# Kernel tuning notes

Hardware: AMD Instinct MI355X
Metric: run time of the kernel (lower is better)

## Reference

```python
import jax, jax.numpy as jnp
import numpy as np

EPS = 1e-5

def _bn2d(x, gamma, beta):
    # training-mode BatchNorm2d: stats over (B, T, F) per channel, biased var
    m = x.mean(axis=(0, 2, 3), keepdims=True)
    v = x.var(axis=(0, 2, 3), keepdims=True)
    return (x - m) * jax.lax.rsqrt(v + EPS) * gamma[None, :, None, None] + beta[None, :, None, None]

def _gn1(x, gamma, beta):
    # GroupNorm(num_groups=1) on (B, C, T): stats over (C, T) per sample
    m = x.mean(axis=(1, 2), keepdims=True)
    v = x.var(axis=(1, 2), keepdims=True)
    return (x - m) * jax.lax.rsqrt(v + EPS) * gamma[None, :, None] + beta[None, :, None]

def _nearest(x, size):
    # torch F.interpolate(mode='nearest') on last dim: src = floor(dst * L_in / L_out)
    L = x.shape[-1]
    idx = jnp.floor(jnp.arange(size) * (L / size)).astype(jnp.int32)
    return x[..., idx]


def setup_inputs() -> dict:
    key = jax.random.key(0)
    ks = jax.random.split(key, 16)
    B, Ca, T, Fa = 2, 512, 256, 128
    Tv = 64
    d = {
        "audio": jax.random.normal(ks[0], (B, Ca, T, Fa), dtype=jnp.float32),
        "video_emb": jax.random.normal(ks[1], (B, Ca, Tv), dtype=jnp.float32),
        # value_conv: depthwise 1x1 Conv2d (no bias) + BatchNorm2d
        "value_w": jax.random.normal(ks[2], (Ca,), dtype=jnp.float32) * 0.1 + 1.0,
        "value_gamma": jax.random.normal(ks[3], (Ca,), dtype=jnp.float32) * 0.1 + 1.0,
        "value_beta": jax.random.normal(ks[4], (Ca,), dtype=jnp.float32) * 0.1,
        # gate_conv: depthwise 1x1 Conv2d (no bias) + BatchNorm2d + ReLU
        "gate_w": jax.random.normal(ks[5], (Ca,), dtype=jnp.float32) * 0.1 + 1.0,
        "gate_gamma": jax.random.normal(ks[6], (Ca,), dtype=jnp.float32) * 0.1 + 1.0,
        "gate_beta": jax.random.normal(ks[7], (Ca,), dtype=jnp.float32) * 0.1,
        # attention_conv: depthwise Conv1d (bias) + GroupNorm(1)
        "att_w": jax.random.normal(ks[8], (Ca,), dtype=jnp.float32) * 0.1 + 1.0,
        "att_b": jax.random.normal(ks[9], (Ca,), dtype=jnp.float32) * 0.1,
        "att_gamma": jax.random.normal(ks[10], (Ca,), dtype=jnp.float32) * 0.1 + 1.0,
        "att_beta": jax.random.normal(ks[11], (Ca,), dtype=jnp.float32) * 0.1,
        # resize_conv: depthwise Conv1d (bias) + GroupNorm(1)
        "res_w": jax.random.normal(ks[12], (Ca,), dtype=jnp.float32) * 0.1 + 1.0,
        "res_b": jax.random.normal(ks[13], (Ca,), dtype=jnp.float32) * 0.1,
        "res_gamma": jax.random.normal(ks[14], (Ca,), dtype=jnp.float32) * 0.1 + 1.0,
        "res_beta": jax.random.normal(ks[15], (Ca,), dtype=jnp.float32) * 0.1,
    }
    return d


def reference(audio, video_emb, value_w, value_gamma, value_beta,
              gate_w, gate_gamma, gate_beta,
              att_w, att_b, att_gamma, att_beta,
              res_w, res_b, res_gamma, res_beta):
    T = audio.shape[2]
    # value branch: depthwise 1x1 conv (per-channel scale) + BN
    a_v = _bn2d(audio * value_w[None, :, None, None], value_gamma, value_beta)  # (B,Ca,T,Fa)
    # attention from video: depthwise conv1d + GN(1) + softmax over time + nearest resize
    att = _gn1(video_emb * att_w[None, :, None] + att_b[None, :, None], att_gamma, att_beta)
    att = _nearest(jax.nn.softmax(att, axis=-1), T)  # (B,Ca,T)
    f1 = att[..., None] * a_v
    # gating branch
    vr = _gn1(video_emb * res_w[None, :, None] + res_b[None, :, None], res_gamma, res_beta)
    vi = _nearest(vr, T)[..., None]  # (B,Ca,T,1)
    a_gate = jax.nn.relu(_bn2d(audio * gate_w[None, :, None, None], gate_gamma, gate_beta))
    f2 = a_gate * vi
    return f1 + f2
```

## Files before the change

### kernel.cpp

```cpp
#include <hip/hip_runtime.h>
#include <math.h>

#define EPS 1e-5f

typedef float f32x4 __attribute__((ext_vector_type(4)));

constexpr int B   = 2;
constexpr int Ca  = 512;
constexpr int T   = 256;
constexpr int Fa  = 128;
constexpr int Tv  = 64;
constexpr int CHW = T * Fa;
constexpr int NSTAT = B * CHW;
constexpr int VID_PER_B = Ca * Tv;

constexpr int WS_COEF = 0;
constexpr int WS_PS   = 2048;
constexpr int WS_PS2  = 4096;
constexpr int WS_ATT  = 6144;
constexpr int WS_VR   = WS_ATT + B * VID_PER_B;

__global__ __launch_bounds__(256) void k_stats(
    const float* __restrict__ audio, float* __restrict__ ws)
{
    const int blk = blockIdx.x;
    const int tid = threadIdx.x;
    const f32x4* a4 = reinterpret_cast<const f32x4*>(audio) + (size_t)blk * 4096;

    float s = 0.f, s2 = 0.f;
    #pragma unroll
    for (int k = 0; k < 16; ++k) {
        f32x4 v = a4[tid + k * 256];
        s  += v.x + v.y + v.z + v.w;
        s2 += v.x * v.x + v.y * v.y + v.z * v.z + v.w * v.w;
    }
    for (int off = 32; off; off >>= 1) {
        s  += __shfl_xor(s,  off);
        s2 += __shfl_xor(s2, off);
    }
    __shared__ float ls[4], ls2[4];
    const int wid = tid >> 6;
    if ((tid & 63) == 0) { ls[wid] = s; ls2[wid] = s2; }
    __syncthreads();
    if (tid == 0) {
        ws[WS_PS  + blk] = ls[0]  + ls[1]  + ls[2]  + ls[3];
        ws[WS_PS2 + blk] = ls2[0] + ls2[1] + ls2[2] + ls2[3];
    }
}

__global__ __launch_bounds__(1024) void k_video(
    const float* __restrict__ video,
    const float* __restrict__ vw, const float* __restrict__ vg, const float* __restrict__ vb,
    const float* __restrict__ gw, const float* __restrict__ gg, const float* __restrict__ gb,
    const float* __restrict__ aw, const float* __restrict__ ab,
    const float* __restrict__ ag, const float* __restrict__ abeta,
    const float* __restrict__ rw, const float* __restrict__ rb,
    const float* __restrict__ rg, const float* __restrict__ rbeta,
    float* __restrict__ ws)
{
    const int b   = blockIdx.x;
    const int tid = threadIdx.x;

    if (b == 0 && tid < Ca) {
        const int c = tid;
        const float S  = ws[WS_PS  + c*2] + ws[WS_PS  + c*2 + 1]
                       + ws[WS_PS  + 1024 + c*2] + ws[WS_PS  + 1024 + c*2 + 1];
        const float S2 = ws[WS_PS2 + c*2] + ws[WS_PS2 + c*2 + 1]
                       + ws[WS_PS2 + 1024 + c*2] + ws[WS_PS2 + 1024 + c*2 + 1];
        const float inv  = 1.f / (float)NSTAT;
        const float mean = S * inv;
        const float var  = S2 * inv - mean * mean;

        float w  = vw[c];
        float sv = w * rsqrtf(w * w * var + EPS) * vg[c];
        ws[WS_COEF + c]        = sv;
        ws[WS_COEF + 512 + c]  = vb[c] - mean * sv;

        w = gw[c];
        float sg = w * rsqrtf(w * w * var + EPS) * gg[c];
        ws[WS_COEF + 1024 + c] = sg;
        ws[WS_COEF + 1536 + c] = gb[c] - mean * sg;
    }

    const int t  = tid & 63;
    const int cl = tid >> 6;
    const float* vbase = video + (size_t)b * VID_PER_B;
    float* att_out = ws + WS_ATT;
    float* vr_out  = ws + WS_VR;

    float s1a = 0.f, s2a = 0.f, s1r = 0.f, s2r = 0.f;
    #pragma unroll
    for (int i = 0; i < Ca / 16; ++i) {
        const int c = cl + 16 * i;
        float v  = vbase[c * Tv + t];
        float xa = v * aw[c] + ab[c];
        float xr = v * rw[c] + rb[c];
        s1a += xa; s2a += xa * xa;
        s1r += xr; s2r += xr * xr;
    }
    for (int off = 32; off; off >>= 1) {
        s1a += __shfl_xor(s1a, off); s2a += __shfl_xor(s2a, off);
        s1r += __shfl_xor(s1r, off); s2r += __shfl_xor(s2r, off);
    }
    __shared__ float red[4][16];
    __shared__ float stats[4];
    const int wid = tid >> 6;
    if ((tid & 63) == 0) {
        red[0][wid] = s1a; red[1][wid] = s2a;
        red[2][wid] = s1r; red[3][wid] = s2r;
    }
    __syncthreads();
    if (tid == 0) {
        float S1a = 0, S2a = 0, S1r = 0, S2r = 0;
        for (int i = 0; i < 16; ++i) {
            S1a += red[0][i]; S2a += red[1][i];
            S1r += red[2][i]; S2r += red[3][i];
        }
        const float inv = 1.f / (float)VID_PER_B;
        float ma = S1a * inv, va = S2a * inv - ma * ma;
        float mr = S1r * inv, vv = S2r * inv - mr * mr;
        stats[0] = ma; stats[1] = rsqrtf(va + EPS);
        stats[2] = mr; stats[3] = rsqrtf(vv + EPS);
    }
    __syncthreads();
    const float ma = stats[0], rsa = stats[1];
    const float mr = stats[2], rsr = stats[3];

    #pragma unroll
    for (int i = 0; i < Ca / 16; ++i) {
        const int c = cl + 16 * i;
        float v  = vbase[c * Tv + t];
        float xa = (v * aw[c] + ab[c] - ma) * rsa * ag[c] + abeta[c];
        float xr = (v * rw[c] + rb[c] - mr) * rsr * rg[c] + rbeta[c];

        float m = xa;
        for (int off = 32; off; off >>= 1) m = fmaxf(m, __shfl_xor(m, off));
        float e = expf(xa - m);
        float sum = e;
        for (int off = 32; off; off >>= 1) sum += __shfl_xor(sum, off);

        const size_t idx = (size_t)b * VID_PER_B + (size_t)c * Tv + t;
        att_out[idx] = e / sum;
        vr_out[idx]  = xr;
    }
}

__global__ __launch_bounds__(256) void k_fuse(
    const float* __restrict__ audio,
    const float* __restrict__ ws,
    float* __restrict__ out)
{
    const int blk = blockIdx.x;
    const int tid = threadIdx.x;
    const f32x4* a4 = reinterpret_cast<const f32x4*>(audio);
    f32x4*       o4 = reinterpret_cast<f32x4*>(out);

    const size_t bc = (size_t)(blk >> 3);
    const int    c  = (int)(bc & (size_t)(Ca - 1));
    const int    t_base = (blk & 7) * 32;

    const float sv = ws[WS_COEF + c];
    const float bv = ws[WS_COEF + 512 + c];
    const float sg = ws[WS_COEF + 1024 + c];
    const float bg = ws[WS_COEF + 1536 + c];
    const float* att = ws + WS_ATT + bc * Tv;
    const float* vr  = ws + WS_VR  + bc * Tv;

    #pragma unroll
    for (int k = 0; k < 4; ++k) {
        const size_t i = (size_t)blk * 1024 + tid + (size_t)k * 256;
        const int    t = t_base + k * 8 + (tid >> 5);
        const float av = att[t >> 2];
        const float vv = vr[t >> 2];

        f32x4 a = a4[i];
        f32x4 r;
        r.x = av * (a.x * sv + bv) + fmaxf(a.x * sg + bg, 0.f) * vv;
        r.y = av * (a.y * sv + bv) + fmaxf(a.y * sg + bg, 0.f) * vv;
        r.z = av * (a.z * sv + bv) + fmaxf(a.z * sg + bg, 0.f) * vv;
        r.w = av * (a.w * sv + bv) + fmaxf(a.w * sg + bg, 0.f) * vv;
        __builtin_nontemporal_store(r, &o4[i]);
    }
}

extern "C" void kernel_launch(void* const* d_in, const int* in_sizes, int n_in,
                              void* d_out, int out_size, void* d_ws, size_t ws_size,
                              hipStream_t stream) {
    const float* audio   = (const float*)d_in[0];
    const float* video   = (const float*)d_in[1];
    const float* value_w = (const float*)d_in[2];
    const float* value_g = (const float*)d_in[3];
    const float* value_b = (const float*)d_in[4];
    const float* gate_w  = (const float*)d_in[5];
    const float* gate_g  = (const float*)d_in[6];
    const float* gate_b  = (const float*)d_in[7];
    const float* att_w   = (const float*)d_in[8];
    const float* att_b   = (const float*)d_in[9];
    const float* att_g   = (const float*)d_in[10];
    const float* att_be  = (const float*)d_in[11];
    const float* res_w   = (const float*)d_in[12];
    const float* res_b   = (const float*)d_in[13];
    const float* res_g   = (const float*)d_in[14];
    const float* res_be  = (const float*)d_in[15];

    float* ws = (float*)d_ws;

    k_stats<<<2048, 256, 0, stream>>>(audio, ws);
    k_video<<<B, 1024, 0, stream>>>(video,
                                    value_w, value_g, value_b,
                                    gate_w, gate_g, gate_b,
                                    att_w, att_b, att_g, att_be,
                                    res_w, res_b, res_g, res_be, ws);
    const int blocks = B * Ca * T * Fa / 4 / 1024;
    k_fuse<<<blocks, 256, 0, stream>>>(audio, ws, (float*)d_out);
}
```

Baseline: 316.3 us.

## Merge stats and video kernels into one launch, fold BN coefficients into fuse

The audio partial-sum kernel and the video attention kernel are combined into one grid of 2050 blocks, with the last two blocks handling the video branch at 256 threads instead of 1024. Computing the BN scale and shift moves into the fuse kernel, so every block recomputes its channel coefficients from the partial sums and the separate per-channel coefficient pass goes away. The audio load in the fuse kernel becomes a nontemporal load. This saves one launch and its serialization, but the video blocks may now finish last with fewer threads, and the nontemporal load may lose L2 reuse of audio read during stats.

```diff
diff --git a/kernel.cpp b/kernel.cpp
--- a/kernel.cpp
+++ b/kernel.cpp
@@ -14,74 +14,48 @@
 constexpr int NSTAT = B * CHW;
 constexpr int VID_PER_B = Ca * Tv;
 
-constexpr int WS_COEF = 0;
-constexpr int WS_PS   = 2048;
-constexpr int WS_PS2  = 4096;
-constexpr int WS_ATT  = 6144;
+constexpr int WS_PS   = 0;
+constexpr int WS_PS2  = 2048;
+constexpr int WS_ATT  = 4096;
 constexpr int WS_VR   = WS_ATT + B * VID_PER_B;
 
-__global__ __launch_bounds__(256) void k_stats(
-    const float* __restrict__ audio, float* __restrict__ ws)
-{
-    const int blk = blockIdx.x;
-    const int tid = threadIdx.x;
-    const f32x4* a4 = reinterpret_cast<const f32x4*>(audio) + (size_t)blk * 4096;
-
-    float s = 0.f, s2 = 0.f;
-    #pragma unroll
-    for (int k = 0; k < 16; ++k) {
-        f32x4 v = a4[tid + k * 256];
-        s  += v.x + v.y + v.z + v.w;
-        s2 += v.x * v.x + v.y * v.y + v.z * v.z + v.w * v.w;
-    }
-    for (int off = 32; off; off >>= 1) {
-        s  += __shfl_xor(s,  off);
-        s2 += __shfl_xor(s2, off);
-    }
-    __shared__ float ls[4], ls2[4];
-    const int wid = tid >> 6;
-    if ((tid & 63) == 0) { ls[wid] = s; ls2[wid] = s2; }
-    __syncthreads();
-    if (tid == 0) {
-        ws[WS_PS  + blk] = ls[0]  + ls[1]  + ls[2]  + ls[3];
-        ws[WS_PS2 + blk] = ls2[0] + ls2[1] + ls2[2] + ls2[3];
-    }
-}
-
-__global__ __launch_bounds__(1024) void k_video(
+__global__ __launch_bounds__(256) void k_pre(
+    const float* __restrict__ audio,
     const float* __restrict__ video,
-    const float* __restrict__ vw, const float* __restrict__ vg, const float* __restrict__ vb,
-    const float* __restrict__ gw, const float* __restrict__ gg, const float* __restrict__ gb,
     const float* __restrict__ aw, const float* __restrict__ ab,
     const float* __restrict__ ag, const float* __restrict__ abeta,
     const float* __restrict__ rw, const float* __restrict__ rb,
     const float* __restrict__ rg, const float* __restrict__ rbeta,
     float* __restrict__ ws)
 {
-    const int b   = blockIdx.x;
+    const int blk = blockIdx.x;
     const int tid = threadIdx.x;
+    __shared__ float sh[17];
 
-    if (b == 0 && tid < Ca) {
-        const int c = tid;
-        const float S  = ws[WS_PS  + c*2] + ws[WS_PS  + c*2 + 1]
-                       + ws[WS_PS  + 1024 + c*2] + ws[WS_PS  + 1024 + c*2 + 1];
-        const float S2 = ws[WS_PS2 + c*2] + ws[WS_PS2 + c*2 + 1]
-                       + ws[WS_PS2 + 1024 + c*2] + ws[WS_PS2 + 1024 + c*2 + 1];
-        const float inv  = 1.f / (float)NSTAT;
-        const float mean = S * inv;
-        const float var  = S2 * inv - mean * mean;
-
-        float w  = vw[c];
-        float sv = w * rsqrtf(w * w * var + EPS) * vg[c];
-        ws[WS_COEF + c]        = sv;
-        ws[WS_COEF + 512 + c]  = vb[c] - mean * sv;
-
-        w = gw[c];
-        float sg = w * rsqrtf(w * w * var + EPS) * gg[c];
-        ws[WS_COEF + 1024 + c] = sg;
-        ws[WS_COEF + 1536 + c] = gb[c] - mean * sg;
+    if (blk < 2048) {
+        const f32x4* a4 = reinterpret_cast<const f32x4*>(audio) + (size_t)blk * 4096;
+        float s = 0.f, s2 = 0.f;
+        #pragma unroll
+        for (int k = 0; k < 16; ++k) {
+            f32x4 v = a4[tid + k * 256];
+            s  += v.x + v.y + v.z + v.w;
+            s2 += v.x * v.x + v.y * v.y + v.z * v.z + v.w * v.w;
+        }
+        for (int off = 32; off; off >>= 1) {
+            s  += __shfl_xor(s,  off);
+            s2 += __shfl_xor(s2, off);
+        }
+        const int wid = tid >> 6;
+        if ((tid & 63) == 0) { sh[wid] = s; sh[4 + wid] = s2; }
+        __syncthreads();
+        if (tid == 0) {
+            ws[WS_PS  + blk] = sh[0] + sh[1] + sh[2] + sh[3];
+            ws[WS_PS2 + blk] = sh[4] + sh[5] + sh[6] + sh[7];
+        }
+        return;
     }
 
+    const int b  = blk - 2048;
     const int t  = tid & 63;
     const int cl = tid >> 6;
     const float* vbase = video + (size_t)b * VID_PER_B;
@@ -89,9 +63,9 @@
     float* vr_out  = ws + WS_VR;
 
     float s1a = 0.f, s2a = 0.f, s1r = 0.f, s2r = 0.f;
-    #pragma unroll
-    for (int i = 0; i < Ca / 16; ++i) {
-        const int c = cl + 16 * i;
+    #pragma unroll 8
+    for (int i = 0; i < Ca / 4; ++i) {
+        const int c = cl + 4 * i;
         float v  = vbase[c * Tv + t];
         float xa = v * aw[c] + ab[c];
         float xr = v * rw[c] + rb[c];
@@ -102,33 +76,30 @@
         s1a += __shfl_xor(s1a, off); s2a += __shfl_xor(s2a, off);
         s1r += __shfl_xor(s1r, off); s2r += __shfl_xor(s2r, off);
     }
-    __shared__ float red[4][16];
-    __shared__ float stats[4];
     const int wid = tid >> 6;
     if ((tid & 63) == 0) {
-        red[0][wid] = s1a; red[1][wid] = s2a;
-        red[2][wid] = s1r; red[3][wid] = s2r;
+        sh[wid]      = s1a; sh[4 + wid]  = s2a;
+        sh[8 + wid]  = s1r; sh[12 + wid] = s2r;
     }
     __syncthreads();
     if (tid == 0) {
-        float S1a = 0, S2a = 0, S1r = 0, S2r = 0;
-        for (int i = 0; i < 16; ++i) {
-            S1a += red[0][i]; S2a += red[1][i];
-            S1r += red[2][i]; S2r += red[3][i];
-        }
+        float S1a = sh[0] + sh[1] + sh[2] + sh[3];
+        float S2a = sh[4] + sh[5] + sh[6] + sh[7];
+        float S1r = sh[8] + sh[9] + sh[10] + sh[11];
+        float S2r = sh[12] + sh[13] + sh[14] + sh[15];
         const float inv = 1.f / (float)VID_PER_B;
         float ma = S1a * inv, va = S2a * inv - ma * ma;
         float mr = S1r * inv, vv = S2r * inv - mr * mr;
-        stats[0] = ma; stats[1] = rsqrtf(va + EPS);
-        stats[2] = mr; stats[3] = rsqrtf(vv + EPS);
+        sh[0] = ma; sh[1] = rsqrtf(va + EPS);
+        sh[2] = mr; sh[3] = rsqrtf(vv + EPS);
     }
     __syncthreads();
-    const float ma = stats[0], rsa = stats[1];
-    const float mr = stats[2], rsr = stats[3];
+    const float ma = sh[0], rsa = sh[1];
+    const float mr = sh[2], rsr = sh[3];
 
-    #pragma unroll
-    for (int i = 0; i < Ca / 16; ++i) {
-        const int c = cl + 16 * i;
+    #pragma unroll 8
+    for (int i = 0; i < Ca / 4; ++i) {
+        const int c = cl + 4 * i;
         float v  = vbase[c * Tv + t];
         float xa = (v * aw[c] + ab[c] - ma) * rsa * ag[c] + abeta[c];
         float xr = (v * rw[c] + rb[c] - mr) * rsr * rg[c] + rbeta[c];
@@ -148,6 +119,8 @@
 __global__ __launch_bounds__(256) void k_fuse(
     const float* __restrict__ audio,
     const float* __restrict__ ws,
+    const float* __restrict__ vw, const float* __restrict__ vg, const float* __restrict__ vb,
+    const float* __restrict__ gw, const float* __restrict__ gg, const float* __restrict__ gb,
     float* __restrict__ out)
 {
     const int blk = blockIdx.x;
@@ -159,10 +132,20 @@
     const int    c  = (int)(bc & (size_t)(Ca - 1));
     const int    t_base = (blk & 7) * 32;
 
-    const float sv = ws[WS_COEF + c];
-    const float bv = ws[WS_COEF + 512 + c];
-    const float sg = ws[WS_COEF + 1024 + c];
-    const float bg = ws[WS_COEF + 1536 + c];
+    const float* ps  = ws + WS_PS;
+    const float* ps2 = ws + WS_PS2;
+    const float S  = ps[c * 2]  + ps[c * 2 + 1]  + ps[1024 + c * 2]  + ps[1024 + c * 2 + 1];
+    const float S2 = ps2[c * 2] + ps2[c * 2 + 1] + ps2[1024 + c * 2] + ps2[1024 + c * 2 + 1];
+    const float inv  = 1.f / (float)NSTAT;
+    const float mean = S * inv;
+    const float var  = S2 * inv - mean * mean;
+    float w  = vw[c];
+    const float sv = w * rsqrtf(w * w * var + EPS) * vg[c];
+    const float bv = vb[c] - mean * sv;
+    w = gw[c];
+    const float sg = w * rsqrtf(w * w * var + EPS) * gg[c];
+    const float bg = gb[c] - mean * sg;
+
     const float* att = ws + WS_ATT + bc * Tv;
     const float* vr  = ws + WS_VR  + bc * Tv;
 
@@ -173,7 +156,7 @@
         const float av = att[t >> 2];
         const float vv = vr[t >> 2];
 
-        f32x4 a = a4[i];
+        f32x4 a = __builtin_nontemporal_load(&a4[i]);
         f32x4 r;
         r.x = av * (a.x * sv + bv) + fmaxf(a.x * sg + bg, 0.f) * vv;
         r.y = av * (a.y * sv + bv) + fmaxf(a.y * sg + bg, 0.f) * vv;
@@ -205,12 +188,12 @@
 
     float* ws = (float*)d_ws;
 
-    k_stats<<<2048, 256, 0, stream>>>(audio, ws);
-    k_video<<<B, 1024, 0, stream>>>(video,
-                                    value_w, value_g, value_b,
-                                    gate_w, gate_g, gate_b,
+    k_pre<<<2050, 256, 0, stream>>>(audio, video,
                                     att_w, att_b, att_g, att_be,
                                     res_w, res_b, res_g, res_be, ws);
     const int blocks = B * Ca * T * Fa / 4 / 1024;
-    k_fuse<<<blocks, 256, 0, stream>>>(audio, ws, (float*)d_out);
+    k_fuse<<<blocks, 256, 0, stream>>>(audio, ws,
+                                       value_w, value_g, value_b,
+                                       gate_w, gate_g, gate_b,
+                                       (float*)d_out);
 }
```

Measured after the change: 323.9 us. 2.4% more time.
